# Kernel tuning notes

Measured on AMD Instinct MI355X. Metric: run time of the kernel, lower is better.

## Reference

```python
import jax, jax.numpy as jnp
import numpy as np
import math

B = 4096
D = 768
HID = 256
C_OLD = 100
C_NEW = 100
NUM_CLASSES = 200
EPSILON = 0.05
TAU = 0.1
EPS = 1e-8
NEG_INF = -1e9


def _l2_normalize(x):
    # matches F.normalize(p=2, dim=1, eps=1e-12)
    n = jnp.linalg.norm(x, axis=1, keepdims=True)
    return x / jnp.maximum(n, 1e-12)


def setup_inputs() -> dict:
    key = jax.random.key(0)
    k1, k2, k3, k4, k5, k6, k7 = jax.random.split(key, 7)
    z_u = jax.random.normal(k1, (B, D), dtype=jnp.float32)
    logits = jax.random.normal(k2, (B, NUM_CLASSES), dtype=jnp.float32)
    old_class_indices = jnp.arange(C_OLD, dtype=jnp.int64 if jax.config.jax_enable_x64 else jnp.int32)
    new_class_indices = jnp.arange(C_OLD, C_OLD + C_NEW, dtype=old_class_indices.dtype)
    base_features = jax.random.normal(k3, (B, D), dtype=jnp.float32)
    s = 1.0 / math.sqrt(D)
    f1_w = jax.random.uniform(k4, (HID, D), dtype=jnp.float32, minval=-s, maxval=s)
    f1_b = jax.random.uniform(k5, (HID,), dtype=jnp.float32, minval=-s, maxval=s)
    f2_w = jax.random.uniform(k6, (HID, D), dtype=jnp.float32, minval=-s, maxval=s)
    f2_b = jax.random.uniform(k7, (HID,), dtype=jnp.float32, minval=-s, maxval=s)
    return {"z_u": z_u, "logits": logits, "old_class_indices": old_class_indices,
            "new_class_indices": new_class_indices, "base_features": base_features,
            "f1_w": f1_w, "f1_b": f1_b, "f2_w": f2_w, "f2_b": f2_b}


def reference(z_u, logits, old_class_indices, new_class_indices, base_features,
              f1_w, f1_b, f2_w, f2_b):
    num_old = old_class_indices.shape[0]
    active = jnp.concatenate([old_class_indices, new_class_indices])

    # ---- soft entropy regularization ----
    probs = jax.nn.softmax(logits[:, active], axis=1)   # (B, C_old+C_new)
    mean_probs = probs.mean(axis=0)
    p_old = mean_probs[:num_old].sum()
    p_new = mean_probs[num_old:].sum()
    loss_inter = (p_old * jnp.log(p_old + EPS) + p_new * jnp.log(p_new + EPS)
                  + math.log(2.0))
    p_old_in = mean_probs[:num_old] / (p_old + EPS)
    loss_old_in = jnp.sum(p_old_in * jnp.log(p_old_in + EPS)) + math.log(num_old)
    p_new_in = mean_probs[num_old:] / (p_new + EPS)
    num_new = new_class_indices.shape[0]
    if num_new > 1:
        loss_new_in = jnp.sum(p_new_in * jnp.log(p_new_in + EPS)) + math.log(num_new)
    else:
        loss_new_in = jnp.float32(0.0)
    loss_entropy = loss_inter + loss_old_in + loss_new_in

    # ---- neighborhood mask from frozen base features ----
    base_norm = _l2_normalize(base_features)
    base_sim = base_norm @ base_norm.T                  # (B, B)
    eye = jnp.eye(base_sim.shape[0], dtype=bool)
    mask = (base_sim > EPSILON) & ~eye                  # (B, B) bool

    # ---- contrastive similarities ----
    z_norm = _l2_normalize(z_u)
    sim = z_norm @ z_norm.T                             # (B, B)

    f1_z = z_u @ f1_w.T + f1_b                          # (B, HID)
    f2_z = z_u @ f2_w.T + f2_b
    attn_logits = jnp.where(mask, f1_z @ f2_z.T, NEG_INF)
    w_ik = jax.nn.softmax(attn_logits, axis=1) * mask.astype(sim.dtype)

    exp_sim = jnp.where(eye, 0.0, jnp.exp(sim / TAU))
    denom = exp_sim.sum(axis=1, keepdims=True)
    log_prob = sim / TAU - jnp.log(denom + EPS)

    num_neighbors = mask.sum(axis=1).astype(sim.dtype)  # (B,)
    valid = num_neighbors > 0
    loss_i = -(w_ik * mask.astype(sim.dtype) * log_prob).sum(axis=1)
    per_sample = jnp.where(valid, loss_i / jnp.maximum(num_neighbors, 1.0), 0.0)
    n_valid = valid.sum().astype(sim.dtype)
    loss_contrastive = jnp.where(n_valid > 0,
                                 per_sample.sum() / jnp.maximum(n_valid, 1.0),
                                 0.0)

    total_loss = loss_entropy + loss_contrastive
    return total_loss
```

## Files before the change

### kernel.cpp

```cpp
#include <hip/hip_runtime.h>
#include <hip/hip_fp8.h>


#define B_N   4096
#define D_N   768
#define HID_N 256
#define NCLS  200
#define NJOBS 1056u

typedef __attribute__((ext_vector_type(8))) short v8s;
typedef __attribute__((ext_vector_type(4))) short v4ss;
typedef __attribute__((ext_vector_type(4))) float v4f;

__device__ __forceinline__ unsigned short f2bf(float x) {
    unsigned int u = __float_as_uint(x);
    unsigned int r = (u + 0x7FFFu + ((u >> 16) & 1u)) >> 16;
    return (unsigned short)r;
}
__device__ __forceinline__ unsigned char f2fp8(float x) {
    __hip_fp8_e4m3 v(x);
    return (unsigned char)v.__x;
}
__device__ __forceinline__ unsigned int pack4fp8(float a, float b, float c, float d) {
    return (unsigned int)f2fp8(a) | ((unsigned int)f2fp8(b) << 8) |
           ((unsigned int)f2fp8(c) << 16) | ((unsigned int)f2fp8(d) << 24);
}

__device__ __forceinline__ void gld16c(const unsigned char* g, unsigned char* l) {
    __builtin_amdgcn_global_load_lds(
        (__attribute__((address_space(1))) void*)g,
        (__attribute__((address_space(3))) void*)l, 16, 0, 0);
}

#define ZERO_ACC24(a) { _Pragma("unroll") for (int _i = 0; _i < 2; _i++) \
    _Pragma("unroll") for (int _j = 0; _j < 4; _j++) a[_i][_j] = (v4f){0.f,0.f,0.f,0.f}; }

__global__ __launch_bounds__(256) void pre_all(
    const float* __restrict__ z, const float* __restrict__ base,
    const float* __restrict__ w1, const float* __restrict__ w2,
    const float* __restrict__ b1, const float* __restrict__ b2,
    const float* __restrict__ logits, const int* __restrict__ oldi,
    const int* __restrict__ newi,
    unsigned char* __restrict__ zn8, unsigned char* __restrict__ bn8,
    unsigned char* __restrict__ f1z8, unsigned char* __restrict__ f2z8,
    float* __restrict__ mpart, float* __restrict__ accums)
{
    __shared__ __align__(16) unsigned char shmem[2 * 64 * 72 * 2];
    int tid = threadIdx.x;

    if (blockIdx.x < 512) {
        unsigned short* Al = (unsigned short*)shmem;
        unsigned short* Bl = Al + 64 * 72;
        int f = blockIdx.x;
        int which = f >> 8;
        int t6 = f & 255;
        int mBase = (t6 >> 2) * 64;
        int nBase = (t6 & 3) * 64;
        const float* wsrc = which ? w2 : w1;
        const float* bias = which ? b2 : b1;
        unsigned char* outz = which ? f2z8 : f1z8;
        int lane = tid & 63, wave = tid >> 6, quad = lane >> 4, col = lane & 15;
        v4f acc[4];
        #pragma unroll
        for (int i = 0; i < 4; i++) acc[i] = (v4f){0.f, 0.f, 0.f, 0.f};
        for (int kc = 0; kc < D_N; kc += 64) {
            __syncthreads();
            #pragma unroll
            for (int s = 0; s < 4; s++) {
                int slot = s * 256 + tid;
                int row = slot >> 4, k4 = slot & 15;
                float4 va = *(const float4*)(z + (size_t)(mBase + row) * D_N + kc + k4 * 4);
                float4 vb = *(const float4*)(wsrc + (size_t)(nBase + row) * D_N + kc + k4 * 4);
                v4ss sa, sb;
                sa[0] = (short)f2bf(va.x); sa[1] = (short)f2bf(va.y);
                sa[2] = (short)f2bf(va.z); sa[3] = (short)f2bf(va.w);
                sb[0] = (short)f2bf(vb.x); sb[1] = (short)f2bf(vb.y);
                sb[2] = (short)f2bf(vb.z); sb[3] = (short)f2bf(vb.w);
                *(v4ss*)(Al + row * 72 + k4 * 4) = sa;
                *(v4ss*)(Bl + row * 72 + k4 * 4) = sb;
            }
            __syncthreads();
            #pragma unroll
            for (int kk = 0; kk < 2; kk++) {
                v8s af = *(const v8s*)(Al + (wave * 16 + col) * 72 + kk * 32 + quad * 8);
                #pragma unroll
                for (int tc = 0; tc < 4; tc++) {
                    v8s bf = *(const v8s*)(Bl + (tc * 16 + col) * 72 + kk * 32 + quad * 8);
                    acc[tc] = __builtin_amdgcn_mfma_f32_16x16x32_bf16(af, bf, acc[tc], 0, 0, 0);
                }
            }
        }
        #pragma unroll
        for (int tc = 0; tc < 4; tc++) {
            int gcol = nBase + tc * 16 + col;
            float bv = bias[gcol];
            #pragma unroll
            for (int reg = 0; reg < 4; reg++) {
                int grow = mBase + wave * 16 + quad * 4 + reg;
                int sw8 = ((grow >> 3) & 1) << 3;
                outz[(size_t)grow * HID_N + (gcol ^ sw8)] =
                    f2fp8(4.0f * (acc[tc][reg] + bv));
            }
        }
        return;
    }
    if (blockIdx.x < 768) {
        int* act = (int*)shmem;
        float* accs = (float*)(shmem + 1024);
        int sb = blockIdx.x - 512;
        int lane = tid & 63, wave = tid >> 6;
        if (sb == 0 && tid < 6) accums[tid] = 0.0f;
        if (tid < NCLS) act[tid] = (tid < 100) ? oldi[tid] : newi[tid - 100];
        accs[tid] = 0.f; accs[256 + tid] = 0.f; accs[512 + tid] = 0.f; accs[768 + tid] = 0.f;
        __syncthreads();
        int a0 = act[lane], a1 = act[lane + 64], a2 = act[lane + 128];
        int a3 = (lane < 8) ? act[lane + 192] : 0;
        int r0 = sb * 16 + wave * 4;
        float c0 = 0.f, c1 = 0.f, c2 = 0.f, c3 = 0.f;
        for (int i = 0; i < 4; i++) {
            const float* lr = logits + (size_t)(r0 + i) * NCLS;
            float x0 = lr[a0], x1 = lr[a1], x2 = lr[a2];
            float x3 = (lane < 8) ? lr[a3] : -3.0e38f;
            float m = fmaxf(fmaxf(x0, x1), fmaxf(x2, x3));
            #pragma unroll
            for (int s = 32; s > 0; s >>= 1) m = fmaxf(m, __shfl_xor(m, s));
            float e0 = __expf(x0 - m), e1 = __expf(x1 - m), e2 = __expf(x2 - m);
            float e3 = (lane < 8) ? __expf(x3 - m) : 0.f;
            float sm = e0 + e1 + e2 + e3;
            #pragma unroll
            for (int s = 32; s > 0; s >>= 1) sm += __shfl_xor(sm, s);
            float inv = 1.0f / sm;
            c0 += e0 * inv; c1 += e1 * inv; c2 += e2 * inv; c3 += e3 * inv;
        }
        accs[wave * 256 + lane] = c0; accs[wave * 256 + lane + 64] = c1;
        accs[wave * 256 + lane + 128] = c2;
        if (lane < 8) accs[wave * 256 + lane + 192] = c3;
        __syncthreads();
        mpart[(size_t)tid * 256 + sb] =
            accs[tid] + accs[256 + tid] + accs[512 + tid] + accs[768 + tid];
        return;
    }
    {
        int nb = blockIdx.x - 768;
        int lane = tid & 63, wave = tid >> 6;
        #pragma unroll
        for (int rr = 0; rr < 2; rr++) {
            int row = nb * 8 + rr * 4 + wave;
            const float* zr = z    + (size_t)row * D_N;
            const float* br = base + (size_t)row * D_N;
            float4 zv0 = *(const float4*)(zr + (size_t)lane * 4);
            float4 zv1 = *(const float4*)(zr + (size_t)(lane + 64) * 4);
            float4 zv2 = *(const float4*)(zr + (size_t)(lane + 128) * 4);
            float4 bv0 = *(const float4*)(br + (size_t)lane * 4);
            float4 bv1 = *(const float4*)(br + (size_t)(lane + 64) * 4);
            float4 bv2 = *(const float4*)(br + (size_t)(lane + 128) * 4);
            float s1 = zv0.x*zv0.x + zv0.y*zv0.y + zv0.z*zv0.z + zv0.w*zv0.w
                     + zv1.x*zv1.x + zv1.y*zv1.y + zv1.z*zv1.z + zv1.w*zv1.w
                     + zv2.x*zv2.x + zv2.y*zv2.y + zv2.z*zv2.z + zv2.w*zv2.w;
            float s2 = bv0.x*bv0.x + bv0.y*bv0.y + bv0.z*bv0.z + bv0.w*bv0.w
                     + bv1.x*bv1.x + bv1.y*bv1.y + bv1.z*bv1.z + bv1.w*bv1.w
                     + bv2.x*bv2.x + bv2.y*bv2.y + bv2.z*bv2.z + bv2.w*bv2.w;
            #pragma unroll
            for (int m = 32; m > 0; m >>= 1) {
                s1 += __shfl_xor(s1, m);
                s2 += __shfl_xor(s2, m);
            }
            float sc1 = 16.0f / fmaxf(sqrtf(s1), 1e-12f);
            float sc2 = 16.0f / fmaxf(sqrtf(s2), 1e-12f);
            size_t o = (size_t)row * D_N;
            int sw8 = ((row >> 3) & 1) << 3;
            *(unsigned int*)(zn8 + o + (((lane      ) * 4) ^ sw8)) =
                pack4fp8(zv0.x*sc1, zv0.y*sc1, zv0.z*sc1, zv0.w*sc1);
            *(unsigned int*)(zn8 + o + (((lane +  64) * 4) ^ sw8)) =
                pack4fp8(zv1.x*sc1, zv1.y*sc1, zv1.z*sc1, zv1.w*sc1);
            *(unsigned int*)(zn8 + o + (((lane + 128) * 4) ^ sw8)) =
                pack4fp8(zv2.x*sc1, zv2.y*sc1, zv2.z*sc1, zv2.w*sc1);
            *(unsigned int*)(bn8 + o + (((lane      ) * 4) ^ sw8)) =
                pack4fp8(bv0.x*sc2, bv0.y*sc2, bv0.z*sc2, bv0.w*sc2);
            *(unsigned int*)(bn8 + o + (((lane +  64) * 4) ^ sw8)) =
                pack4fp8(bv1.x*sc2, bv1.y*sc2, bv1.z*sc2, bv1.w*sc2);
            *(unsigned int*)(bn8 + o + (((lane + 128) * 4) ^ sw8)) =
                pack4fp8(bv2.x*sc2, bv2.y*sc2, bv2.z*sc2, bv2.w*sc2);
        }
    }
}

__global__ __launch_bounds__(256, 2) void main_fused(
    const unsigned char* __restrict__ zn8, const unsigned char* __restrict__ bn8,
    const unsigned char* __restrict__ f1z8, const unsigned char* __restrict__ f2z8,
    float* __restrict__ partials, int* __restrict__ jobcnt)
{
    __shared__ __align__(16) unsigned char S[53248];
    __shared__ int sh_j;
    unsigned char* SA_B = S;
    unsigned char* SA_S = S + 8192;
    unsigned char* SB_B = S + 16384;
    unsigned char* SB_S = S + 32768;
    unsigned char* F1   = S;
    unsigned char* F2   = S + 16384;
    float4* red = (float4*)(S + 49152);

    int tid = threadIdx.x, lane = tid & 63, wave = tid >> 6;
    int quad = lane >> 4, col = lane & 15;
    int wr3 = wave >> 1, wc3 = wave & 1;
    const int r8 = lane >> 3;
    const int kbl8 = (lane & 7) ^ r8;
    const int sub8 = ((quad & 1) ^ (col >> 3)) << 3;

    for (;;) {
        __syncthreads();
        if (tid == 0) sh_j = atomicAdd(jobcnt, 1);
        __syncthreads();
        unsigned int j = (unsigned int)sh_j;
        if (j >= NJOBS) return;

        int ib, jc, h; bool diag;
        if (j < 992u) {
            int pp = (int)(j >> 1); h = (int)(j & 1u); diag = false;
            int t = (int)((1.0f + sqrtf(8.0f * (float)pp + 1.0f)) * 0.5f);
            t = (t < 1) ? 1 : ((t > 31) ? 31 : t);
            while (t > 1  && t * (t - 1) / 2 > pp) --t;
            while (t < 31 && (t + 1) * t / 2 <= pp) ++t;
            jc = t; ib = pp - t * (t - 1) / 2;
        } else {
            int dd = (int)(j - 992u); ib = jc = dd >> 1; h = dd & 1; diag = true;
        }
        int aRow0 = ib * 128 + h * 64;
        int bRow0 = jc * 128;

        v4f accB[2][4], accS[2][4];
        ZERO_ACC24(accB); ZERO_ACC24(accS);
        for (int kc = 0; kc < D_N; kc += 128) {
            __syncthreads();
            #pragma unroll
            for (int s = 0; s < 4; s++) {
                int rowbase = s * 32 + wave * 8;
                size_t gOff = (size_t)(bRow0 + rowbase + r8) * D_N + kc + kbl8 * 16;
                gld16c(bn8 + gOff, SB_B + rowbase * 128);
                gld16c(zn8 + gOff, SB_S + rowbase * 128);
            }
            if (!diag) {
                #pragma unroll
                for (int s = 0; s < 2; s++) {
                    int rowbase = s * 32 + wave * 8;
                    size_t gOff = (size_t)(aRow0 + rowbase + r8) * D_N + kc + kbl8 * 16;
                    gld16c(bn8 + gOff, SA_B + rowbase * 128);
                    gld16c(zn8 + gOff, SA_S + rowbase * 128);
                }
            }
            __syncthreads();
            const unsigned char* AB = diag ? (SB_B + h * 64 * 128) : SA_B;
            const unsigned char* AS = diag ? (SB_S + h * 64 * 128) : SA_S;
            #pragma unroll
            for (int kk = 0; kk < 4; kk++) {
                int gbase = kk * 2 + (quad >> 1);
                int off = ((gbase ^ (col & 7)) << 4) + sub8;
                long a1[2], a2[2], b1[4], b2[4];
                #pragma unroll
                for (int t = 0; t < 2; t++) {
                    int rA = (wr3 * 32 + t * 16 + col) * 128;
                    a1[t] = *(const long*)(AB + rA + off);
                    a2[t] = *(const long*)(AS + rA + off);
                }
                #pragma unroll
                for (int t = 0; t < 4; t++) {
                    int rB = (wc3 * 64 + t * 16 + col) * 128;
                    b1[t] = *(const long*)(SB_B + rB + off);
                    b2[t] = *(const long*)(SB_S + rB + off);
                }
                #pragma unroll
                for (int tr = 0; tr < 2; tr++)
                    #pragma unroll
                    for (int tc = 0; tc < 4; tc++) {
                        accB[tr][tc] = __builtin_amdgcn_mfma_f32_16x16x32_fp8_fp8(
                            a1[tr], b1[tc], accB[tr][tc], 0, 0, 0);
                        accS[tr][tc] = __builtin_amdgcn_mfma_f32_16x16x32_fp8_fp8(
                            a2[tr], b2[tc], accS[tr][tc], 0, 0, 0);
                    }
            }
        }

        __syncthreads();
        {
            int r4 = lane >> 4;
            #pragma unroll
            for (int s = 0; s < 8; s++) {
                int rowbase = s * 16 + wave * 4;
                int row = rowbase + r4;
                int kb = (lane & 15) ^ (row & 15);
                gld16c(f2z8 + (size_t)(bRow0 + row) * HID_N + kb * 16, F2 + rowbase * 256);
            }
            #pragma unroll
            for (int s = 0; s < 4; s++) {
                int rowbase = s * 16 + wave * 4;
                int row = rowbase + r4;
                int kb = (lane & 15) ^ (row & 15);
                gld16c(f1z8 + (size_t)(aRow0 + row) * HID_N + kb * 16, F1 + rowbase * 256);
            }
        }

        unsigned int mb = 0u;
        #pragma unroll
        for (int tr = 0; tr < 2; tr++)
            #pragma unroll
            for (int tc = 0; tc < 4; tc++)
                #pragma unroll
                for (int reg = 0; reg < 4; reg++) {
                    int grow = aRow0 + wr3 * 32 + tr * 16 + quad * 4 + reg;
                    int gcol = bRow0 + wc3 * 64 + tc * 16 + col;
                    if (accB[tr][tc][reg] > 12.8f && grow != gcol)
                        mb |= 1u << (tr * 16 + tc * 4 + reg);
                }

        v4f accA[2][4]; ZERO_ACC24(accA);
        __syncthreads();
        #pragma unroll
        for (int kk = 0; kk < 8; kk++) {
            int gbase = kk * 2 + (quad >> 1);
            int off = ((gbase ^ col) << 4) + sub8;
            long af[2], bf[4];
            #pragma unroll
            for (int t = 0; t < 2; t++)
                af[t] = *(const long*)(F1 + (wr3 * 32 + t * 16 + col) * 256 + off);
            #pragma unroll
            for (int t = 0; t < 4; t++)
                bf[t] = *(const long*)(F2 + (wc3 * 64 + t * 16 + col) * 256 + off);
            #pragma unroll
            for (int tr = 0; tr < 2; tr++)
                #pragma unroll
                for (int tc = 0; tc < 4; tc++)
                    accA[tr][tc] = __builtin_amdgcn_mfma_f32_16x16x32_fp8_fp8(
                        af[tr], bf[tc], accA[tr][tc], 0, 0, 0);
        }

        __syncthreads();
        if (!diag) {
            int r4 = lane >> 4;
            #pragma unroll
            for (int s = 0; s < 8; s++) {
                int rowbase = s * 16 + wave * 4;
                int row = rowbase + r4;
                int kb = (lane & 15) ^ (row & 15);
                gld16c(f1z8 + (size_t)(bRow0 + row) * HID_N + kb * 16, F2 + rowbase * 256);
            }
            #pragma unroll
            for (int s = 0; s < 4; s++) {
                int rowbase = s * 16 + wave * 4;
                int row = rowbase + r4;
                int kb = (lane & 15) ^ (row & 15);
                gld16c(f2z8 + (size_t)(aRow0 + row) * HID_N + kb * 16, F1 + rowbase * 256);
            }
        }

        #pragma unroll
        for (int tr = 0; tr < 2; tr++) {
            float ls[4], as[4], nn[4], ds[4];
            #pragma unroll
            for (int r = 0; r < 4; r++) { ls[r]=0.f; as[r]=0.f; nn[r]=0.f; ds[r]=0.f; }
            #pragma unroll
            for (int tc = 0; tc < 4; tc++)
                #pragma unroll
                for (int reg = 0; reg < 4; reg++) {
                    float sv = accS[tr][tc][reg] * 0.00390625f;
                    int grow = aRow0 + wr3 * 32 + tr * 16 + quad * 4 + reg;
                    int gcol = bRow0 + wc3 * 64 + tc * 16 + col;
                    if (grow != gcol) ds[reg] += __expf(sv * 10.0f);
                    if ((mb >> (tr * 16 + tc * 4 + reg)) & 1u) {
                        float e = __expf(accA[tr][tc][reg] * 0.0625f);
                        ls[reg] += e; as[reg] += e * sv; nn[reg] += 1.f;
                    }
                }
            #pragma unroll
            for (int r = 0; r < 4; r++) {
                #pragma unroll
                for (int m = 1; m < 16; m <<= 1) {
                    ls[r] += __shfl_xor(ls[r], m);
                    as[r] += __shfl_xor(as[r], m);
                    ds[r] += __shfl_xor(ds[r], m);
                    nn[r] += __shfl_xor(nn[r], m);
                }
                if (col == 0) {
                    int row = aRow0 + wr3 * 32 + tr * 16 + quad * 4 + r;
                    float4 v; v.x = ls[r]; v.y = as[r]; v.z = ds[r]; v.w = nn[r];
                    *(float4*)(partials + ((size_t)row * 64 + jc * 2 + wc3) * 4) = v;
                }
            }
        }

        if (!diag) {
            ZERO_ACC24(accA);
            __syncthreads();
            #pragma unroll
            for (int kk = 0; kk < 8; kk++) {
                int gbase = kk * 2 + (quad >> 1);
                int off = ((gbase ^ col) << 4) + sub8;
                long af[2], bf[4];
                #pragma unroll
                for (int t = 0; t < 2; t++)
                    af[t] = *(const long*)(F1 + (wr3 * 32 + t * 16 + col) * 256 + off);
                #pragma unroll
                for (int t = 0; t < 4; t++)
                    bf[t] = *(const long*)(F2 + (wc3 * 64 + t * 16 + col) * 256 + off);
                #pragma unroll
                for (int tr = 0; tr < 2; tr++)
                    #pragma unroll
                    for (int tc = 0; tc < 4; tc++)
                        accA[tr][tc] = __builtin_amdgcn_mfma_f32_16x16x32_fp8_fp8(
                            af[tr], bf[tc], accA[tr][tc], 0, 0, 0);
            }
            #pragma unroll
            for (int tc = 0; tc < 4; tc++) {
                float l2 = 0.f, a2 = 0.f, d2 = 0.f, n2 = 0.f;
                #pragma unroll
                for (int tr = 0; tr < 2; tr++)
                    #pragma unroll
                    for (int reg = 0; reg < 4; reg++) {
                        float sv = accS[tr][tc][reg] * 0.00390625f;
                        d2 += __expf(sv * 10.0f);
                        if ((mb >> (tr * 16 + tc * 4 + reg)) & 1u) {
                            float e = __expf(accA[tr][tc][reg] * 0.0625f);
                            l2 += e; a2 += e * sv; n2 += 1.f;
                        }
                    }
                #pragma unroll
                for (int m = 16; m < 64; m <<= 1) {
                    l2 += __shfl_xor(l2, m);
                    a2 += __shfl_xor(a2, m);
                    d2 += __shfl_xor(d2, m);
                    n2 += __shfl_xor(n2, m);
                }
                if (lane < 16) {
                    float4 v; v.x = l2; v.y = a2; v.z = d2; v.w = n2;
                    red[wr3 * 128 + wc3 * 64 + tc * 16 + lane] = v;
                }
            }
            __syncthreads();
            if (tid < 128) {
                float4 u = red[tid], v = red[128 + tid];
                float4 w; w.x = u.x + v.x; w.y = u.y + v.y;
                w.z = u.z + v.z; w.w = u.w + v.w;
                *(float4*)(partials + ((size_t)(bRow0 + tid) * 64 + ib * 2 + h) * 4) = w;
            }
        }
    }
}

__global__ __launch_bounds__(256) void row_reduce_fin(
    const float* __restrict__ partials, const float* __restrict__ mpart,
    float* __restrict__ acc, float* __restrict__ out)
{
    int tid = threadIdx.x;
    int row = blockIdx.x * 64 + (tid >> 2);
    int sub = tid & 3;
    const float4* p = (const float4*)partials + (size_t)row * 64 + sub * 16;
    float L = 0.f, A = 0.f, Dn = 0.f, NN = 0.f;
    #pragma unroll
    for (int c = 0; c < 16; c++) { float4 v = p[c]; L += v.x; A += v.y; Dn += v.z; NN += v.w; }
    #pragma unroll
    for (int m = 1; m < 4; m <<= 1) {
        L += __shfl_xor(L, m); A += __shfl_xor(A, m);
        Dn += __shfl_xor(Dn, m); NN += __shfl_xor(NN, m);
    }
    float per = 0.f, val = 0.f;
    if (sub == 0 && NN > 0.5f) {
        per = (logf(Dn + 1e-8f) - 10.0f * (A / L)) / NN;
        val = 1.0f;
    }
    __shared__ float red[256];
    __shared__ float r2s[256];
    __shared__ int amLast;
    red[tid] = per; r2s[tid] = val; __syncthreads();
    for (int s = 128; s > 0; s >>= 1) {
        if (tid < s) { red[tid] += red[tid + s]; r2s[tid] += r2s[tid + s]; }
        __syncthreads();
    }
    if (tid == 0) {
        atomicAdd(&acc[0], red[0]);
        atomicAdd(&acc[1], r2s[0]);
        __threadfence();
        int old = atomicAdd((int*)&acc[2], 1);
        amLast = (old == (int)gridDim.x - 1);
    }
    __syncthreads();
    if (!amLast) return;

    __shared__ float bcast[2];
    float pcl = 0.0f;
    if (tid < NCLS) {
        const float4* mp = (const float4*)(mpart + (size_t)tid * 256);
        float s = 0.f;
        #pragma unroll
        for (int c = 0; c < 64; c++) { float4 v = mp[c]; s += v.x + v.y + v.z + v.w; }
        pcl = s * (1.0f / 4096.0f);
    }
    red[tid] = (tid < 100) ? pcl : 0.0f; __syncthreads();
    for (int s = 128; s > 0; s >>= 1) { if (tid < s) red[tid] += red[tid + s]; __syncthreads(); }
    if (tid == 0) bcast[0] = red[0];
    __syncthreads();
    red[tid] = (tid >= 100 && tid < NCLS) ? pcl : 0.0f; __syncthreads();
    for (int s = 128; s > 0; s >>= 1) { if (tid < s) red[tid] += red[tid + s]; __syncthreads(); }
    if (tid == 0) bcast[1] = red[0];
    __syncthreads();
    float p_old = bcast[0], p_new = bcast[1];

    float t = 0.0f;
    if (tid < 100)       { float q = pcl / (p_old + 1e-8f); t = q * logf(q + 1e-8f); }
    else if (tid < NCLS) { float q = pcl / (p_new + 1e-8f); t = q * logf(q + 1e-8f); }
    red[tid] = t; __syncthreads();
    for (int s = 128; s > 0; s >>= 1) { if (tid < s) red[tid] += red[tid + s]; __syncthreads(); }

    if (tid == 0) {
        float s0 = __hip_atomic_load(&acc[0], __ATOMIC_RELAXED, __HIP_MEMORY_SCOPE_AGENT);
        float s1 = __hip_atomic_load(&acc[1], __ATOMIC_RELAXED, __HIP_MEMORY_SCOPE_AGENT);
        float loss_inter = p_old * logf(p_old + 1e-8f) + p_new * logf(p_new + 1e-8f)
                           + 0.69314718056f;
        float loss_entropy = loss_inter + red[0] + 2.0f * 4.60517018599f;
        float lc = (s1 > 0.5f) ? s0 / s1 : 0.0f;
        out[0] = loss_entropy + lc;
    }
}

extern "C" void kernel_launch(void* const* d_in, const int* in_sizes, int n_in,
                              void* d_out, int out_size, void* d_ws, size_t ws_size,
                              hipStream_t stream)
{
    const float* z_u    = (const float*)d_in[0];
    const float* logits = (const float*)d_in[1];
    const int*   oldi   = (const int*)d_in[2];
    const int*   newi   = (const int*)d_in[3];
    const float* basef  = (const float*)d_in[4];
    const float* f1w    = (const float*)d_in[5];
    const float* f1b    = (const float*)d_in[6];
    const float* f2w    = (const float*)d_in[7];
    const float* f2b    = (const float*)d_in[8];
    float* out = (float*)d_out;

    unsigned char* zn8   = (unsigned char*)d_ws;
    unsigned char* bn8   = zn8 + (size_t)B_N * D_N;
    unsigned char* f1z8  = bn8 + (size_t)B_N * D_N;
    unsigned char* f2z8  = f1z8 + (size_t)B_N * HID_N;
    float* partials = (float*)(f2z8 + (size_t)B_N * HID_N);
    float* mpart    = partials + (size_t)B_N * 64 * 4;
    float* accums   = mpart + 256 * 256;
    int*   jobcnt   = (int*)(accums + 4);

    pre_all<<<512 + 256 + 512, 256, 0, stream>>>(
        z_u, basef, f1w, f2w, f1b, f2b, logits, oldi, newi,
        zn8, bn8, f1z8, f2z8, mpart, accums);
    main_fused<<<512, 256, 0, stream>>>(zn8, bn8, f1z8, f2z8, partials, jobcnt);
    row_reduce_fin<<<64, 256, 0, stream>>>(partials, mpart, accums, out);
}
```

Baseline: 168.7 us.

## Fuse three kernels into one persistent kernel with grid-wide spin barriers

Merges the preprocessing, main pairwise-similarity, and row-reduction/finalize kernels into a single 512-block persistent kernel. Each block does one GEMM tile, a logits-softmax slice for half the blocks, and a normalization slice, then all blocks meet at an atomic spin barrier before pulling work from the job queue. A second counter picks the last 64 blocks to do the row reduction and finalize. This removes two kernel launches and their gaps, but relies on all 512 blocks being resident at once and adds a memset launch plus the cost of spinning at the barrier.

```diff
diff --git a/kernel.cpp b/kernel.cpp
--- a/kernel.cpp
+++ b/kernel.cpp
@@ -7,6 +7,7 @@
 #define HID_N 256
 #define NCLS  200
 #define NJOBS 1056u
+#define NBLK  512
 
 typedef __attribute__((ext_vector_type(8))) short v8s;
 typedef __attribute__((ext_vector_type(4))) short v4ss;
@@ -25,7 +26,6 @@
     return (unsigned int)f2fp8(a) | ((unsigned int)f2fp8(b) << 8) |
            ((unsigned int)f2fp8(c) << 16) | ((unsigned int)f2fp8(d) << 24);
 }
-
 __device__ __forceinline__ void gld16c(const unsigned char* g, unsigned char* l) {
     __builtin_amdgcn_global_load_lds(
         (__attribute__((address_space(1))) void*)g,
@@ -35,7 +35,15 @@
 #define ZERO_ACC24(a) { _Pragma("unroll") for (int _i = 0; _i < 2; _i++) \
     _Pragma("unroll") for (int _j = 0; _j < 4; _j++) a[_i][_j] = (v4f){0.f,0.f,0.f,0.f}; }
 
-__global__ __launch_bounds__(256) void pre_all(
+__device__ __forceinline__ void spin_until(int* cnt, int want) {
+    int it = 0;
+    while (__hip_atomic_load(cnt, __ATOMIC_ACQUIRE, __HIP_MEMORY_SCOPE_AGENT) < want) {
+        __builtin_amdgcn_s_sleep(16);
+        if (++it > (1 << 22)) break;
+    }
+}
+
+__global__ __launch_bounds__(256, 2) void fused_all(
     const float* __restrict__ z, const float* __restrict__ base,
     const float* __restrict__ w1, const float* __restrict__ w2,
     const float* __restrict__ b1, const float* __restrict__ b2,
@@ -43,15 +51,21 @@
     const int* __restrict__ newi,
     unsigned char* __restrict__ zn8, unsigned char* __restrict__ bn8,
     unsigned char* __restrict__ f1z8, unsigned char* __restrict__ f2z8,
-    float* __restrict__ mpart, float* __restrict__ accums)
+    float* __restrict__ partials, float* __restrict__ mpart,
+    float* __restrict__ accums, float* __restrict__ out)
 {
-    __shared__ __align__(16) unsigned char shmem[2 * 64 * 72 * 2];
-    int tid = threadIdx.x;
-
-    if (blockIdx.x < 512) {
-        unsigned short* Al = (unsigned short*)shmem;
+    __shared__ __align__(16) unsigned char S[53248];
+    __shared__ int sh_i;
+    __shared__ int sh_last;
+    int* cbase = (int*)accums;
+
+    int tid = threadIdx.x, bid = blockIdx.x;
+    int lane = tid & 63, wave = tid >> 6, quad = lane >> 4, col = lane & 15;
+
+    {
+        unsigned short* Al = (unsigned short*)S;
         unsigned short* Bl = Al + 64 * 72;
-        int f = blockIdx.x;
+        int f = bid;
         int which = f >> 8;
         int t6 = f & 255;
         int mBase = (t6 >> 2) * 64;
@@ -59,7 +73,6 @@
         const float* wsrc = which ? w2 : w1;
         const float* bias = which ? b2 : b1;
         unsigned char* outz = which ? f2z8 : f1z8;
-        int lane = tid & 63, wave = tid >> 6, quad = lane >> 4, col = lane & 15;
         v4f acc[4];
         #pragma unroll
         for (int i = 0; i < 4; i++) acc[i] = (v4f){0.f, 0.f, 0.f, 0.f};
@@ -102,14 +115,13 @@
                     f2fp8(4.0f * (acc[tc][reg] + bv));
             }
         }
-        return;
-    }
-    if (blockIdx.x < 768) {
-        int* act = (int*)shmem;
-        float* accs = (float*)(shmem + 1024);
-        int sb = blockIdx.x - 512;
-        int lane = tid & 63, wave = tid >> 6;
-        if (sb == 0 && tid < 6) accums[tid] = 0.0f;
+    }
+    __syncthreads();
+
+    if (bid < 256) {
+        int* act = (int*)S;
+        float* accs = (float*)(S + 1024);
+        int sb = bid;
         if (tid < NCLS) act[tid] = (tid < 100) ? oldi[tid] : newi[tid - 100];
         accs[tid] = 0.f; accs[256 + tid] = 0.f; accs[512 + tid] = 0.f; accs[768 + tid] = 0.f;
         __syncthreads();
@@ -138,11 +150,11 @@
         __syncthreads();
         mpart[(size_t)tid * 256 + sb] =
             accs[tid] + accs[256 + tid] + accs[512 + tid] + accs[768 + tid];
-        return;
-    }
+    }
+    __syncthreads();
+
     {
-        int nb = blockIdx.x - 768;
-        int lane = tid & 63, wave = tid >> 6;
+        int nb = (bid < 256) ? (256 + bid) : (bid - 256);
         #pragma unroll
         for (int rr = 0; rr < 2; rr++) {
             int row = nb * 8 + rr * 4 + wave;
@@ -183,212 +195,135 @@
                 pack4fp8(bv2.x*sc2, bv2.y*sc2, bv2.z*sc2, bv2.w*sc2);
         }
     }
-}
-
-__global__ __launch_bounds__(256, 2) void main_fused(
-    const unsigned char* __restrict__ zn8, const unsigned char* __restrict__ bn8,
-    const unsigned char* __restrict__ f1z8, const unsigned char* __restrict__ f2z8,
-    float* __restrict__ partials, int* __restrict__ jobcnt)
-{
-    __shared__ __align__(16) unsigned char S[53248];
-    __shared__ int sh_j;
-    unsigned char* SA_B = S;
-    unsigned char* SA_S = S + 8192;
-    unsigned char* SB_B = S + 16384;
-    unsigned char* SB_S = S + 32768;
-    unsigned char* F1   = S;
-    unsigned char* F2   = S + 16384;
-    float4* red = (float4*)(S + 49152);
-
-    int tid = threadIdx.x, lane = tid & 63, wave = tid >> 6;
-    int quad = lane >> 4, col = lane & 15;
-    int wr3 = wave >> 1, wc3 = wave & 1;
-    const int r8 = lane >> 3;
-    const int kbl8 = (lane & 7) ^ r8;
-    const int sub8 = ((quad & 1) ^ (col >> 3)) << 3;
-
-    for (;;) {
-        __syncthreads();
-        if (tid == 0) sh_j = atomicAdd(jobcnt, 1);
-        __syncthreads();
-        unsigned int j = (unsigned int)sh_j;
-        if (j >= NJOBS) return;
-
-        int ib, jc, h; bool diag;
-        if (j < 992u) {
-            int pp = (int)(j >> 1); h = (int)(j & 1u); diag = false;
-            int t = (int)((1.0f + sqrtf(8.0f * (float)pp + 1.0f)) * 0.5f);
-            t = (t < 1) ? 1 : ((t > 31) ? 31 : t);
-            while (t > 1  && t * (t - 1) / 2 > pp) --t;
-            while (t < 31 && (t + 1) * t / 2 <= pp) ++t;
-            jc = t; ib = pp - t * (t - 1) / 2;
-        } else {
-            int dd = (int)(j - 992u); ib = jc = dd >> 1; h = dd & 1; diag = true;
-        }
-        int aRow0 = ib * 128 + h * 64;
-        int bRow0 = jc * 128;
-
-        v4f accB[2][4], accS[2][4];
-        ZERO_ACC24(accB); ZERO_ACC24(accS);
-        for (int kc = 0; kc < D_N; kc += 128) {
-            __syncthreads();
-            #pragma unroll
-            for (int s = 0; s < 4; s++) {
-                int rowbase = s * 32 + wave * 8;
-                size_t gOff = (size_t)(bRow0 + rowbase + r8) * D_N + kc + kbl8 * 16;
-                gld16c(bn8 + gOff, SB_B + rowbase * 128);
-                gld16c(zn8 + gOff, SB_S + rowbase * 128);
-            }
-            if (!diag) {
-                #pragma unroll
-                for (int s = 0; s < 2; s++) {
+
+    __threadfence();
+    __syncthreads();
+    if (tid == 0) {
+        __hip_atomic_fetch_add(&cbase[3], 1, __ATOMIC_ACQ_REL, __HIP_MEMORY_SCOPE_AGENT);
+        spin_until(&cbase[3], NBLK);
+    }
+    __syncthreads();
+    __threadfence();
+
+    {
+        unsigned char* SA_B = S;
+        unsigned char* SA_S = S + 8192;
+        unsigned char* SB_B = S + 16384;
+        unsigned char* SB_S = S + 32768;
+        unsigned char* F1   = S;
+        unsigned char* F2   = S + 16384;
+        float4* red = (float4*)(S + 49152);
+        int wr3 = wave >> 1, wc3 = wave & 1;
+        const int r8 = lane >> 3;
+        const int kbl8 = (lane & 7) ^ r8;
+        const int sub8 = ((quad & 1) ^ (col >> 3)) << 3;
+
+        for (;;) {
+            __syncthreads();
+            if (tid == 0) sh_i = atomicAdd(&cbase[4], 1);
+            __syncthreads();
+            unsigned int j = (unsigned int)sh_i;
+            if (j >= NJOBS) break;
+
+            int ib, jc, h; bool diag;
+            if (j < 992u) {
+                int pp = (int)(j >> 1); h = (int)(j & 1u); diag = false;
+                int t = (int)((1.0f + sqrtf(8.0f * (float)pp + 1.0f)) * 0.5f);
+                t = (t < 1) ? 1 : ((t > 31) ? 31 : t);
+                while (t > 1  && t * (t - 1) / 2 > pp) --t;
+                while (t < 31 && (t + 1) * t / 2 <= pp) ++t;
+                jc = t; ib = pp - t * (t - 1) / 2;
+            } else {
+                int dd = (int)(j - 992u); ib = jc = dd >> 1; h = dd & 1; diag = true;
+            }
+            int aRow0 = ib * 128 + h * 64;
+            int bRow0 = jc * 128;
+
+            v4f accB[2][4], accS[2][4];
+            ZERO_ACC24(accB); ZERO_ACC24(accS);
+            for (int kc = 0; kc < D_N; kc += 128) {
+                __syncthreads();
+                #pragma unroll
+                for (int s = 0; s < 4; s++) {
                     int rowbase = s * 32 + wave * 8;
-                    size_t gOff = (size_t)(aRow0 + rowbase + r8) * D_N + kc + kbl8 * 16;
-                    gld16c(bn8 + gOff, SA_B + rowbase * 128);
-                    gld16c(zn8 + gOff, SA_S + rowbase * 128);
-                }
-            }
-            __syncthreads();
-            const unsigned char* AB = diag ? (SB_B + h * 64 * 128) : SA_B;
-            const unsigned char* AS = diag ? (SB_S + h * 64 * 128) : SA_S;
-            #pragma unroll
-            for (int kk = 0; kk < 4; kk++) {
-                int gbase = kk * 2 + (quad >> 1);
-                int off = ((gbase ^ (col & 7)) << 4) + sub8;
-                long a1[2], a2[2], b1[4], b2[4];
-                #pragma unroll
-                for (int t = 0; t < 2; t++) {
-                    int rA = (wr3 * 32 + t * 16 + col) * 128;
-                    a1[t] = *(const long*)(AB + rA + off);
-                    a2[t] = *(const long*)(AS + rA + off);
-                }
-                #pragma unroll
-                for (int t = 0; t < 4; t++) {
-                    int rB = (wc3 * 64 + t * 16 + col) * 128;
-                    b1[t] = *(const long*)(SB_B + rB + off);
-                    b2[t] = *(const long*)(SB_S + rB + off);
-                }
-                #pragma unroll
-                for (int tr = 0; tr < 2; tr++)
-                    #pragma unroll
-                    for (int tc = 0; tc < 4; tc++) {
-                        accB[tr][tc] = __builtin_amdgcn_mfma_f32_16x16x32_fp8_fp8(
-                            a1[tr], b1[tc], accB[tr][tc], 0, 0, 0);
-                        accS[tr][tc] = __builtin_amdgcn_mfma_f32_16x16x32_fp8_fp8(
-                            a2[tr], b2[tc], accS[tr][tc], 0, 0, 0);
-                    }
-            }
-        }
-
-        __syncthreads();
-        {
-            int r4 = lane >> 4;
-            #pragma unroll
-            for (int s = 0; s < 8; s++) {
-                int rowbase = s * 16 + wave * 4;
-                int row = rowbase + r4;
-                int kb = (lane & 15) ^ (row & 15);
-                gld16c(f2z8 + (size_t)(bRow0 + row) * HID_N + kb * 16, F2 + rowbase * 256);
-            }
-            #pragma unroll
-            for (int s = 0; s < 4; s++) {
-                int rowbase = s * 16 + wave * 4;
-                int row = rowbase + r4;
-                int kb = (lane & 15) ^ (row & 15);
-                gld16c(f1z8 + (size_t)(aRow0 + row) * HID_N + kb * 16, F1 + rowbase * 256);
-            }
-        }
-
-        unsigned int mb = 0u;
-        #pragma unroll
-        for (int tr = 0; tr < 2; tr++)
-            #pragma unroll
-            for (int tc = 0; tc < 4; tc++)
-                #pragma unroll
-                for (int reg = 0; reg < 4; reg++) {
-                    int grow = aRow0 + wr3 * 32 + tr * 16 + quad * 4 + reg;
-                    int gcol = bRow0 + wc3 * 64 + tc * 16 + col;
-                    if (accB[tr][tc][reg] > 12.8f && grow != gcol)
-                        mb |= 1u << (tr * 16 + tc * 4 + reg);
-                }
-
-        v4f accA[2][4]; ZERO_ACC24(accA);
-        __syncthreads();
-        #pragma unroll
-        for (int kk = 0; kk < 8; kk++) {
-            int gbase = kk * 2 + (quad >> 1);
-            int off = ((gbase ^ col) << 4) + sub8;
-            long af[2], bf[4];
-            #pragma unroll
-            for (int t = 0; t < 2; t++)
-                af[t] = *(const long*)(F1 + (wr3 * 32 + t * 16 + col) * 256 + off);
-            #pragma unroll
-            for (int t = 0; t < 4; t++)
-                bf[t] = *(const long*)(F2 + (wc3 * 64 + t * 16 + col) * 256 + off);
+                    size_t gOff = (size_t)(bRow0 + rowbase + r8) * D_N + kc + kbl8 * 16;
+                    gld16c(bn8 + gOff, SB_B + rowbase * 128);
+                    gld16c(zn8 + gOff, SB_S + rowbase * 128);
+                }
+                if (!diag) {
+                    #pragma unroll
+                    for (int s = 0; s < 2; s++) {
+                        int rowbase = s * 32 + wave * 8;
+                        size_t gOff = (size_t)(aRow0 + rowbase + r8) * D_N + kc + kbl8 * 16;
+                        gld16c(bn8 + gOff, SA_B + rowbase * 128);
+                        gld16c(zn8 + gOff, SA_S + rowbase * 128);
+                    }
+                }
+                __syncthreads();
+                const unsigned char* AB = diag ? (SB_B + h * 64 * 128) : SA_B;
+                const unsigned char* AS = diag ? (SB_S + h * 64 * 128) : SA_S;
+                #pragma unroll
+                for (int kk = 0; kk < 4; kk++) {
+                    int gbase = kk * 2 + (quad >> 1);
+                    int off = ((gbase ^ (col & 7)) << 4) + sub8;
+                    long a1[2], a2[2], b1[4], b2[4];
+                    #pragma unroll
+                    for (int t = 0; t < 2; t++) {
+                        int rA = (wr3 * 32 + t * 16 + col) * 128;
+                        a1[t] = *(const long*)(AB + rA + off);
+                        a2[t] = *(const long*)(AS + rA + off);
+                    }
+                    #pragma unroll
+                    for (int t = 0; t < 4; t++) {
+                        int rB = (wc3 * 64 + t * 16 + col) * 128;
+                        b1[t] = *(const long*)(SB_B + rB + off);
+                        b2[t] = *(const long*)(SB_S + rB + off);
+                    }
+                    #pragma unroll
+                    for (int tr = 0; tr < 2; tr++)
+                        #pragma unroll
+                        for (int tc = 0; tc < 4; tc++) {
+                            accB[tr][tc] = __builtin_amdgcn_mfma_f32_16x16x32_fp8_fp8(
+                                a1[tr], b1[tc], accB[tr][tc], 0, 0, 0);
+                            accS[tr][tc] = __builtin_amdgcn_mfma_f32_16x16x32_fp8_fp8(
+                                a2[tr], b2[tc], accS[tr][tc], 0, 0, 0);
+                        }
+                }
+            }
+
+            __syncthreads();
+            {
+                int r4 = lane >> 4;
+                #pragma unroll
+                for (int s = 0; s < 8; s++) {
+                    int rowbase = s * 16 + wave * 4;
+                    int row = rowbase + r4;
+                    int kb = (lane & 15) ^ (row & 15);
+                    gld16c(f2z8 + (size_t)(bRow0 + row) * HID_N + kb * 16, F2 + rowbase * 256);
+                }
+                #pragma unroll
+                for (int s = 0; s < 4; s++) {
+                    int rowbase = s * 16 + wave * 4;
+                    int row = rowbase + r4;
+                    int kb = (lane & 15) ^ (row & 15);
+                    gld16c(f1z8 + (size_t)(aRow0 + row) * HID_N + kb * 16, F1 + rowbase * 256);
+                }
+            }
+
+            unsigned int mb = 0u;
             #pragma unroll
             for (int tr = 0; tr < 2; tr++)
                 #pragma unroll
                 for (int tc = 0; tc < 4; tc++)
-                    accA[tr][tc] = __builtin_amdgcn_mfma_f32_16x16x32_fp8_fp8(
-                        af[tr], bf[tc], accA[tr][tc], 0, 0, 0);
-        }
-
-        __syncthreads();
-        if (!diag) {
-            int r4 = lane >> 4;
-            #pragma unroll
-            for (int s = 0; s < 8; s++) {
-                int rowbase = s * 16 + wave * 4;
-                int row = rowbase + r4;
-                int kb = (lane & 15) ^ (row & 15);
-                gld16c(f1z8 + (size_t)(bRow0 + row) * HID_N + kb * 16, F2 + rowbase * 256);
-            }
-            #pragma unroll
-            for (int s = 0; s < 4; s++) {
-                int rowbase = s * 16 + wave * 4;
-                int row = rowbase + r4;
-                int kb = (lane & 15) ^ (row & 15);
-                gld16c(f2z8 + (size_t)(aRow0 + row) * HID_N + kb * 16, F1 + rowbase * 256);
-            }
-        }
-
-        #pragma unroll
-        for (int tr = 0; tr < 2; tr++) {
-            float ls[4], as[4], nn[4], ds[4];
-            #pragma unroll
-            for (int r = 0; r < 4; r++) { ls[r]=0.f; as[r]=0.f; nn[r]=0.f; ds[r]=0.f; }
-            #pragma unroll
-            for (int tc = 0; tc < 4; tc++)
-                #pragma unroll
-                for (int reg = 0; reg < 4; reg++) {
-                    float sv = accS[tr][tc][reg] * 0.00390625f;
-                    int grow = aRow0 + wr3 * 32 + tr * 16 + quad * 4 + reg;
-                    int gcol = bRow0 + wc3 * 64 + tc * 16 + col;
-                    if (grow != gcol) ds[reg] += __expf(sv * 10.0f);
-                    if ((mb >> (tr * 16 + tc * 4 + reg)) & 1u) {
-                        float e = __expf(accA[tr][tc][reg] * 0.0625f);
-                        ls[reg] += e; as[reg] += e * sv; nn[reg] += 1.f;
-                    }
-                }
-            #pragma unroll
-            for (int r = 0; r < 4; r++) {
-                #pragma unroll
-                for (int m = 1; m < 16; m <<= 1) {
-                    ls[r] += __shfl_xor(ls[r], m);
-                    as[r] += __shfl_xor(as[r], m);
-                    ds[r] += __shfl_xor(ds[r], m);
-                    nn[r] += __shfl_xor(nn[r], m);
-                }
-                if (col == 0) {
-                    int row = aRow0 + wr3 * 32 + tr * 16 + quad * 4 + r;
-                    float4 v; v.x = ls[r]; v.y = as[r]; v.z = ds[r]; v.w = nn[r];
-                    *(float4*)(partials + ((size_t)row * 64 + jc * 2 + wc3) * 4) = v;
-                }
-            }
-        }
-
-        if (!diag) {
-            ZERO_ACC24(accA);
+                    #pragma unroll
+                    for (int reg = 0; reg < 4; reg++) {
+                        int grow = aRow0 + wr3 * 32 + tr * 16 + quad * 4 + reg;
+                        int gcol = bRow0 + wc3 * 64 + tc * 16 + col;
+                        if (accB[tr][tc][reg] > 12.8f && grow != gcol)
+                            mb |= 1u << (tr * 16 + tc * 4 + reg);
+                    }
+
+            v4f accA[2][4]; ZERO_ACC24(accA);
             __syncthreads();
             #pragma unroll
             for (int kk = 0; kk < 8; kk++) {
@@ -408,115 +343,200 @@
                         accA[tr][tc] = __builtin_amdgcn_mfma_f32_16x16x32_fp8_fp8(
                             af[tr], bf[tc], accA[tr][tc], 0, 0, 0);
             }
-            #pragma unroll
-            for (int tc = 0; tc < 4; tc++) {
-                float l2 = 0.f, a2 = 0.f, d2 = 0.f, n2 = 0.f;
-                #pragma unroll
-                for (int tr = 0; tr < 2; tr++)
+
+            __syncthreads();
+            if (!diag) {
+                int r4 = lane >> 4;
+                #pragma unroll
+                for (int s = 0; s < 8; s++) {
+                    int rowbase = s * 16 + wave * 4;
+                    int row = rowbase + r4;
+                    int kb = (lane & 15) ^ (row & 15);
+                    gld16c(f1z8 + (size_t)(bRow0 + row) * HID_N + kb * 16, F2 + rowbase * 256);
+                }
+                #pragma unroll
+                for (int s = 0; s < 4; s++) {
+                    int rowbase = s * 16 + wave * 4;
+                    int row = rowbase + r4;
+                    int kb = (lane & 15) ^ (row & 15);
+                    gld16c(f2z8 + (size_t)(aRow0 + row) * HID_N + kb * 16, F1 + rowbase * 256);
+                }
+            }
+
+            #pragma unroll
+            for (int tr = 0; tr < 2; tr++) {
+                float ls[4], as[4], nn[4], ds[4];
+                #pragma unroll
+                for (int r = 0; r < 4; r++) { ls[r]=0.f; as[r]=0.f; nn[r]=0.f; ds[r]=0.f; }
+                #pragma unroll
+                for (int tc = 0; tc < 4; tc++)
                     #pragma unroll
                     for (int reg = 0; reg < 4; reg++) {
                         float sv = accS[tr][tc][reg] * 0.00390625f;
-                        d2 += __expf(sv * 10.0f);
+                        int grow = aRow0 + wr3 * 32 + tr * 16 + quad * 4 + reg;
+                        int gcol = bRow0 + wc3 * 64 + tc * 16 + col;
+                        if (grow != gcol) ds[reg] += __expf(sv * 10.0f);
                         if ((mb >> (tr * 16 + tc * 4 + reg)) & 1u) {
                             float e = __expf(accA[tr][tc][reg] * 0.0625f);
-                            l2 += e; a2 += e * sv; n2 += 1.f;
+                            ls[reg] += e; as[reg] += e * sv; nn[reg] += 1.f;
                         }
                     }
                 #pragma unroll
-                for (int m = 16; m < 64; m <<= 1) {
-                    l2 += __shfl_xor(l2, m);
-                    a2 += __shfl_xor(a2, m);
-                    d2 += __shfl_xor(d2, m);
-                    n2 += __shfl_xor(n2, m);
-                }
-                if (lane < 16) {
-                    float4 v; v.x = l2; v.y = a2; v.z = d2; v.w = n2;
-                    red[wr3 * 128 + wc3 * 64 + tc * 16 + lane] = v;
-                }
-            }
-            __syncthreads();
-            if (tid < 128) {
-                float4 u = red[tid], v = red[128 + tid];
-                float4 w; w.x = u.x + v.x; w.y = u.y + v.y;
-                w.z = u.z + v.z; w.w = u.w + v.w;
-                *(float4*)(partials + ((size_t)(bRow0 + tid) * 64 + ib * 2 + h) * 4) = w;
-            }
-        }
-    }
-}
-
-__global__ __launch_bounds__(256) void row_reduce_fin(
-    const float* __restrict__ partials, const float* __restrict__ mpart,
-    float* __restrict__ acc, float* __restrict__ out)
-{
-    int tid = threadIdx.x;
-    int row = blockIdx.x * 64 + (tid >> 2);
-    int sub = tid & 3;
-    const float4* p = (const float4*)partials + (size_t)row * 64 + sub * 16;
-    float L = 0.f, A = 0.f, Dn = 0.f, NN = 0.f;
-    #pragma unroll
-    for (int c = 0; c < 16; c++) { float4 v = p[c]; L += v.x; A += v.y; Dn += v.z; NN += v.w; }
-    #pragma unroll
-    for (int m = 1; m < 4; m <<= 1) {
-        L += __shfl_xor(L, m); A += __shfl_xor(A, m);
-        Dn += __shfl_xor(Dn, m); NN += __shfl_xor(NN, m);
-    }
-    float per = 0.f, val = 0.f;
-    if (sub == 0 && NN > 0.5f) {
-        per = (logf(Dn + 1e-8f) - 10.0f * (A / L)) / NN;
-        val = 1.0f;
-    }
-    __shared__ float red[256];
-    __shared__ float r2s[256];
-    __shared__ int amLast;
-    red[tid] = per; r2s[tid] = val; __syncthreads();
-    for (int s = 128; s > 0; s >>= 1) {
-        if (tid < s) { red[tid] += red[tid + s]; r2s[tid] += r2s[tid + s]; }
+                for (int r = 0; r < 4; r++) {
+                    #pragma unroll
+                    for (int m = 1; m < 16; m <<= 1) {
+                        ls[r] += __shfl_xor(ls[r], m);
+                        as[r] += __shfl_xor(as[r], m);
+                        ds[r] += __shfl_xor(ds[r], m);
+                        nn[r] += __shfl_xor(nn[r], m);
+                    }
+                    if (col == 0) {
+                        int row = aRow0 + wr3 * 32 + tr * 16 + quad * 4 + r;
+                        float4 v; v.x = ls[r]; v.y = as[r]; v.z = ds[r]; v.w = nn[r];
+                        *(float4*)(partials + ((size_t)row * 64 + jc * 2 + wc3) * 4) = v;
+                    }
+                }
+            }
+
+            if (!diag) {
+                ZERO_ACC24(accA);
+                __syncthreads();
+                #pragma unroll
+                for (int kk = 0; kk < 8; kk++) {
+                    int gbase = kk * 2 + (quad >> 1);
+                    int off = ((gbase ^ col) << 4) + sub8;
+                    long af[2], bf[4];
+                    #pragma unroll
+                    for (int t = 0; t < 2; t++)
+                        af[t] = *(const long*)(F1 + (wr3 * 32 + t * 16 + col) * 256 + off);
+                    #pragma unroll
+                    for (int t = 0; t < 4; t++)
+                        bf[t] = *(const long*)(F2 + (wc3 * 64 + t * 16 + col) * 256 + off);
+                    #pragma unroll
+                    for (int tr = 0; tr < 2; tr++)
+                        #pragma unroll
+                        for (int tc = 0; tc < 4; tc++)
+                            accA[tr][tc] = __builtin_amdgcn_mfma_f32_16x16x32_fp8_fp8(
+                                af[tr], bf[tc], accA[tr][tc], 0, 0, 0);
+                }
+                #pragma unroll
+                for (int tc = 0; tc < 4; tc++) {
+                    float l2 = 0.f, a2 = 0.f, d2 = 0.f, n2 = 0.f;
+                    #pragma unroll
+                    for (int tr = 0; tr < 2; tr++)
+                        #pragma unroll
+                        for (int reg = 0; reg < 4; reg++) {
+                            float sv = accS[tr][tc][reg] * 0.00390625f;
+                            d2 += __expf(sv * 10.0f);
+                            if ((mb >> (tr * 16 + tc * 4 + reg)) & 1u) {
+                                float e = __expf(accA[tr][tc][reg] * 0.0625f);
+                                l2 += e; a2 += e * sv; n2 += 1.f;
+                            }
+                        }
+                    #pragma unroll
+                    for (int m = 16; m < 64; m <<= 1) {
+                        l2 += __shfl_xor(l2, m);
+                        a2 += __shfl_xor(a2, m);
+                        d2 += __shfl_xor(d2, m);
+                        n2 += __shfl_xor(n2, m);
+                    }
+                    if (lane < 16) {
+                        float4 v; v.x = l2; v.y = a2; v.z = d2; v.w = n2;
+                        red[wr3 * 128 + wc3 * 64 + tc * 16 + lane] = v;
+                    }
+                }
+                __syncthreads();
+                if (tid < 128) {
+                    float4 u = red[tid], v = red[128 + tid];
+                    float4 w; w.x = u.x + v.x; w.y = u.y + v.y;
+                    w.z = u.z + v.z; w.w = u.w + v.w;
+                    *(float4*)(partials + ((size_t)(bRow0 + tid) * 64 + ib * 2 + h) * 4) = w;
+                }
+            }
+        }
+    }
+
+    __threadfence();
+    __syncthreads();
+    if (tid == 0)
+        sh_i = __hip_atomic_fetch_add(&cbase[5], 1, __ATOMIC_ACQ_REL, __HIP_MEMORY_SCOPE_AGENT);
+    __syncthreads();
+    int myslot = sh_i;
+    if (myslot < NBLK - 64) return;
+    if (tid == 0) spin_until(&cbase[5], NBLK);
+    __syncthreads();
+    __threadfence();
+    int slot = myslot - (NBLK - 64);
+
+    {
+        float* rr_red = (float*)S;
+        float* rr_r2s = (float*)(S + 1024);
+        float* rr_bc  = (float*)(S + 2048);
+
+        int row = slot * 64 + (tid >> 2);
+        int sub = tid & 3;
+        const float4* p = (const float4*)partials + (size_t)row * 64 + sub * 16;
+        float L = 0.f, A = 0.f, Dn = 0.f, NN = 0.f;
+        #pragma unroll
+        for (int c = 0; c < 16; c++) { float4 v = p[c]; L += v.x; A += v.y; Dn += v.z; NN += v.w; }
+        #pragma unroll
+        for (int m = 1; m < 4; m <<= 1) {
+            L += __shfl_xor(L, m); A += __shfl_xor(A, m);
+            Dn += __shfl_xor(Dn, m); NN += __shfl_xor(NN, m);
+        }
+        float per = 0.f, val = 0.f;
+        if (sub == 0 && NN > 0.5f) {
+            per = (logf(Dn + 1e-8f) - 10.0f * (A / L)) / NN;
+            val = 1.0f;
+        }
+        rr_red[tid] = per; rr_r2s[tid] = val; __syncthreads();
+        for (int s = 128; s > 0; s >>= 1) {
+            if (tid < s) { rr_red[tid] += rr_red[tid + s]; rr_r2s[tid] += rr_r2s[tid + s]; }
+            __syncthreads();
+        }
+        if (tid == 0) {
+            atomicAdd(&accums[0], rr_red[0]);
+            atomicAdd(&accums[1], rr_r2s[0]);
+            __threadfence();
+            int old = atomicAdd(&cbase[2], 1);
+            sh_last = (old == 63);
+        }
         __syncthreads();
-    }
-    if (tid == 0) {
-        atomicAdd(&acc[0], red[0]);
-        atomicAdd(&acc[1], r2s[0]);
-        __threadfence();
-        int old = atomicAdd((int*)&acc[2], 1);
-        amLast = (old == (int)gridDim.x - 1);
-    }
-    __syncthreads();
-    if (!amLast) return;
-
-    __shared__ float bcast[2];
-    float pcl = 0.0f;
-    if (tid < NCLS) {
-        const float4* mp = (const float4*)(mpart + (size_t)tid * 256);
-        float s = 0.f;
-        #pragma unroll
-        for (int c = 0; c < 64; c++) { float4 v = mp[c]; s += v.x + v.y + v.z + v.w; }
-        pcl = s * (1.0f / 4096.0f);
-    }
-    red[tid] = (tid < 100) ? pcl : 0.0f; __syncthreads();
-    for (int s = 128; s > 0; s >>= 1) { if (tid < s) red[tid] += red[tid + s]; __syncthreads(); }
-    if (tid == 0) bcast[0] = red[0];
-    __syncthreads();
-    red[tid] = (tid >= 100 && tid < NCLS) ? pcl : 0.0f; __syncthreads();
-    for (int s = 128; s > 0; s >>= 1) { if (tid < s) red[tid] += red[tid + s]; __syncthreads(); }
-    if (tid == 0) bcast[1] = red[0];
-    __syncthreads();
-    float p_old = bcast[0], p_new = bcast[1];
-
-    float t = 0.0f;
-    if (tid < 100)       { float q = pcl / (p_old + 1e-8f); t = q * logf(q + 1e-8f); }
-    else if (tid < NCLS) { float q = pcl / (p_new + 1e-8f); t = q * logf(q + 1e-8f); }
-    red[tid] = t; __syncthreads();
-    for (int s = 128; s > 0; s >>= 1) { if (tid < s) red[tid] += red[tid + s]; __syncthreads(); }
-
-    if (tid == 0) {
-        float s0 = __hip_atomic_load(&acc[0], __ATOMIC_RELAXED, __HIP_MEMORY_SCOPE_AGENT);
-        float s1 = __hip_atomic_load(&acc[1], __ATOMIC_RELAXED, __HIP_MEMORY_SCOPE_AGENT);
-        float loss_inter = p_old * logf(p_old + 1e-8f) + p_new * logf(p_new + 1e-8f)
-                           + 0.69314718056f;
-        float loss_entropy = loss_inter + red[0] + 2.0f * 4.60517018599f;
-        float lc = (s1 > 0.5f) ? s0 / s1 : 0.0f;
-        out[0] = loss_entropy + lc;
+        if (!sh_last) return;
+
+        float pcl = 0.0f;
+        if (tid < NCLS) {
+            const float4* mp = (const float4*)(mpart + (size_t)tid * 256);
+            float s = 0.f;
+            #pragma unroll
+            for (int c = 0; c < 64; c++) { float4 v = mp[c]; s += v.x + v.y + v.z + v.w; }
+            pcl = s * (1.0f / 4096.0f);
+        }
+        rr_red[tid] = (tid < 100) ? pcl : 0.0f; __syncthreads();
+        for (int s = 128; s > 0; s >>= 1) { if (tid < s) rr_red[tid] += rr_red[tid + s]; __syncthreads(); }
+        if (tid == 0) rr_bc[0] = rr_red[0];
+        __syncthreads();
+        rr_red[tid] = (tid >= 100 && tid < NCLS) ? pcl : 0.0f; __syncthreads();
+        for (int s = 128; s > 0; s >>= 1) { if (tid < s) rr_red[tid] += rr_red[tid + s]; __syncthreads(); }
+        if (tid == 0) rr_bc[1] = rr_red[0];
+        __syncthreads();
+        float p_old = rr_bc[0], p_new = rr_bc[1];
+
+        float t = 0.0f;
+        if (tid < 100)       { float q = pcl / (p_old + 1e-8f); t = q * logf(q + 1e-8f); }
+        else if (tid < NCLS) { float q = pcl / (p_new + 1e-8f); t = q * logf(q + 1e-8f); }
+        rr_red[tid] = t; __syncthreads();
+        for (int s = 128; s > 0; s >>= 1) { if (tid < s) rr_red[tid] += rr_red[tid + s]; __syncthreads(); }
+
+        if (tid == 0) {
+            float s0 = __hip_atomic_load(&accums[0], __ATOMIC_RELAXED, __HIP_MEMORY_SCOPE_AGENT);
+            float s1 = __hip_atomic_load(&accums[1], __ATOMIC_RELAXED, __HIP_MEMORY_SCOPE_AGENT);
+            float loss_inter = p_old * logf(p_old + 1e-8f) + p_new * logf(p_new + 1e-8f)
+                               + 0.69314718056f;
+            float loss_entropy = loss_inter + rr_red[0] + 2.0f * 4.60517018599f;
+            float lc = (s1 > 0.5f) ? s0 / s1 : 0.0f;
+            out[0] = loss_entropy + lc;
+        }
     }
 }
 
@@ -542,11 +562,9 @@
     float* partials = (float*)(f2z8 + (size_t)B_N * HID_N);
     float* mpart    = partials + (size_t)B_N * 64 * 4;
     float* accums   = mpart + 256 * 256;
-    int*   jobcnt   = (int*)(accums + 4);
-
-    pre_all<<<512 + 256 + 512, 256, 0, stream>>>(
+
+    hipMemsetAsync(accums, 0, 32, stream);
+    fused_all<<<NBLK, 256, 0, stream>>>(
         z_u, basef, f1w, f2w, f1b, f2b, logits, oldi, newi,
-        zn8, bn8, f1z8, f2z8, mpart, accums);
-    main_fused<<<512, 256, 0, stream>>>(zn8, bn8, f1z8, f2z8, partials, jobcnt);
-    row_reduce_fin<<<64, 256, 0, stream>>>(partials, mpart, accums, out);
-}
+        zn8, bn8, f1z8, f2z8, partials, mpart, accums, out);
+}
```

Result: slower. 362.3 us (+114.7%).
